# Performance work log

Hardware: AMD Instinct MI355X
Metric: run time of the kernel (lower is better)

## Reference

```python
import jax, jax.numpy as jnp
import numpy as np

B, S, E, H = 4, 2048, 1024, 16
DH = E // H  # head_dim = 64


def setup_inputs() -> dict:
    key = jax.random.key(0)
    k1, k2, k3 = jax.random.split(key, 3)
    x = jax.random.normal(k1, (B, S, E), dtype=jnp.float32)
    # xavier-uniform-like scale for dense kernels
    Wqkv = jax.random.normal(k2, (E, 3 * E), dtype=jnp.float32) * (1.0 / np.sqrt(E))
    Wout = jax.random.normal(k3, (E, E), dtype=jnp.float32) * (1.0 / np.sqrt(E))
    return {"x": x, "Wqkv": Wqkv, "Wout": Wout}


def reference(x, Wqkv, Wout):
    b, s, e = x.shape
    qkv = jnp.einsum("bse,ef->bsf", x, Wqkv)            # [B,S,3E]
    qkv = qkv.reshape(b, s, H, 3 * DH).transpose(0, 2, 1, 3)  # [B,H,S,3*DH]
    q, k, v = jnp.split(qkv, 3, axis=-1)                # each [B,H,S,DH]
    scale = 1.0 / jnp.sqrt(jnp.asarray(DH, dtype=x.dtype))
    scores = jnp.einsum("bhqd,bhkd->bhqk", q, k) * scale  # [B,H,S,S] materialized
    attn = jax.nn.softmax(scores, axis=-1)
    values = jnp.einsum("bhqk,bhkd->bhqd", attn, v)     # [B,H,S,DH]
    values = values.transpose(0, 2, 1, 3).reshape(b, s, e)
    out = jnp.einsum("bse,ef->bsf", values, Wout)       # [B,S,E]
    return out
```

## Files before the change

### kernel.cpp

```cpp
#include <hip/hip_runtime.h>

typedef __attribute__((ext_vector_type(8))) __bf16 bf16x8;
typedef __attribute__((ext_vector_type(4))) float f32x4;

#define LOG2E 1.4426950408889634f
#define QSCALE (0.125f * LOG2E)
#define SMAX_FIXED 13.0f

static __device__ __forceinline__ void gl_lds16(const void* g, void* l) {
  __builtin_amdgcn_global_load_lds(
      (__attribute__((address_space(1))) void*)(g),
      (__attribute__((address_space(3))) void*)(l), 16, 0, 0);
}

__global__ __launch_bounds__(256) void convert_f32_bf16(const float* __restrict__ in,
                                                        __bf16* __restrict__ out,
                                                        int n8) {
  const int i = blockIdx.x * 256 + threadIdx.x;
  if (i >= n8) return;
  const f32x4 a = *(const f32x4*)(in + (size_t)i * 8);
  const f32x4 b = *(const f32x4*)(in + (size_t)i * 8 + 4);
  bf16x8 o;
#pragma unroll
  for (int j = 0; j < 4; ++j) o[j] = (__bf16)a[j];
#pragma unroll
  for (int j = 0; j < 4; ++j) o[4 + j] = (__bf16)b[j];
  *(bf16x8*)(out + (size_t)i * 8) = o;
}

__global__ __launch_bounds__(256) void transpose_f32_bf16(
    const float* __restrict__ in, __bf16* __restrict__ out, int R, int C) {
  __shared__ __bf16 tile[64][72];
  const int t = threadIdx.x;
  const int c0 = blockIdx.x * 64;
  const int r0 = blockIdx.y * 64;
  const int lr = t >> 2;
  const int lc = (t & 3) * 16;
  const float* src = in + (size_t)(r0 + lr) * C + c0 + lc;
  bf16x8 w0, w1;
#pragma unroll
  for (int j = 0; j < 2; ++j) {
    const f32x4 a = *(const f32x4*)(src + j * 8);
    const f32x4 b = *(const f32x4*)(src + j * 8 + 4);
    bf16x8 o;
#pragma unroll
    for (int k = 0; k < 4; ++k) o[k] = (__bf16)a[k];
#pragma unroll
    for (int k = 0; k < 4; ++k) o[4 + k] = (__bf16)b[k];
    *(bf16x8*)&tile[lr][lc + j * 8] = o;
  }
  __syncthreads();
#pragma unroll
  for (int j = 0; j < 8; ++j) {
    w0[j] = tile[lc + j][lr];
    w1[j] = tile[lc + 8 + j][lr];
  }
  __bf16* dst = out + (size_t)(c0 + lr) * R + r0 + lc;
  *(bf16x8*)dst = w0;
  *(bf16x8*)(dst + 8) = w1;
}

#define FENCEOFF

#define STAGE_A(TT, KH)                                                  \
  do {                                                                   \
    const int kg_ = (TT) * 64 + (KH) * 32;                               \
    char* d_ = lds + ((TT) & 1) * 32768 + (KH) * 16384 + t * 16;         \
    gl_lds16(Ab + g0 + kg_, d_);                                         \
    gl_lds16(Ab + g1 + kg_, d_ + 8192);                                  \
  } while (0)

#define STAGE_B(TT, KH)                                                  \
  do {                                                                   \
    const int kg_ = (TT) * 64 + (KH) * 32;                               \
    char* d_ = lds + 65536 + ((TT) & 1) * 32768 + (KH) * 16384 + t * 16; \
    gl_lds16(Bb + g0 + kg_, d_);                                         \
    gl_lds16(Bb + g1 + kg_, d_ + 8192);                                  \
  } while (0)

#define READ_A(MIH, KK)                                                          \
  do {                                                                           \
    const char* p_ = lds + buf * 32768 + (KK) * 16384 +                          \
                     (wm * 8 + (MIH) * 4) * 1024 + lfo;                          \
    a0 = *(const bf16x8*)p_;                                                     \
    a1 = *(const bf16x8*)(p_ + 1024);                                            \
    a2 = *(const bf16x8*)(p_ + 2048);                                            \
    a3 = *(const bf16x8*)(p_ + 3072);                                            \
  } while (0)

#define READ_B(KK)                                                               \
  do {                                                                           \
    const char* p_ = lds + 65536 + buf * 32768 + (KK) * 16384 + wn * 4096 + lfo; \
    b0 = *(const bf16x8*)p_;                                                     \
    b1 = *(const bf16x8*)(p_ + 1024);                                            \
    b2 = *(const bf16x8*)(p_ + 2048);                                            \
    b3 = *(const bf16x8*)(p_ + 3072);                                            \
  } while (0)

#define MROW(H, MI, AV)                                                          \
  acc[(H) * 4 + (MI)][0] =                                                       \
      __builtin_amdgcn_mfma_f32_16x16x32_bf16(AV, b0, acc[(H) * 4 + (MI)][0], 0, 0, 0); \
  acc[(H) * 4 + (MI)][1] =                                                       \
      __builtin_amdgcn_mfma_f32_16x16x32_bf16(AV, b1, acc[(H) * 4 + (MI)][1], 0, 0, 0); \
  acc[(H) * 4 + (MI)][2] =                                                       \
      __builtin_amdgcn_mfma_f32_16x16x32_bf16(AV, b2, acc[(H) * 4 + (MI)][2], 0, 0, 0); \
  acc[(H) * 4 + (MI)][3] =                                                       \
      __builtin_amdgcn_mfma_f32_16x16x32_bf16(AV, b3, acc[(H) * 4 + (MI)][3], 0, 0, 0);

#define MFMA16(H)                      \
  do {                                 \
    __builtin_amdgcn_s_setprio(1);     \
    MROW(H, 0, a0)                     \
    MROW(H, 1, a1)                     \
    MROW(H, 2, a2)                     \
    MROW(H, 3, a3)                     \
    __builtin_amdgcn_s_setprio(0);     \
  } while (0)

template <int EPI>
__global__ __launch_bounds__(512, 2) void gemm256(
    const __bf16* __restrict__ A, const __bf16* __restrict__ Bt,
    float* __restrict__ Cf, __bf16* __restrict__ q_ws, __bf16* __restrict__ k_ws,
    __bf16* __restrict__ vT_ws, int M, int N, int K) {
  (void)M;
  extern __shared__ char lds[];
  const int t = threadIdx.x;
  const int lane = t & 63;
  const int quad = lane >> 4, l15 = lane & 15;
  const int w = t >> 6;
  const int wm = w >> 2, wn = w & 3;

  const int gx = gridDim.x;
  int lid = blockIdx.y * gx + blockIdx.x;
  lid = (lid & 7) * ((gx * gridDim.y) >> 3) + (lid >> 3);
  const int m0 = (lid % gx) * 256;
  const int n0 = (lid / gx) * 256;

  int rowS[2], kcS[2];
#pragma unroll
  for (int l = 0; l < 2; ++l) {
    const int LB = l * 8192 + t * 16;
    const int r_in = (LB >> 6) & 15;
    const int ch = ((LB >> 5) & 1) ^ ((r_in >> 3) & 1);
    rowS[l] = (LB >> 10) * 16 + r_in;
    kcS[l] = ch * 16 + ((LB >> 4) & 1) * 8;
  }
  const __bf16* Ab = A + (size_t)m0 * K;
  const __bf16* Bb = Bt + (size_t)n0 * K;
  const size_t g0 = (size_t)rowS[0] * K + kcS[0];
  const size_t g1 = (size_t)rowS[1] * K + kcS[1];

  const int lfo = l15 * 64 + ((((quad >> 1) ^ (l15 >> 3)) & 1) << 5) + ((quad & 1) << 4);

  const f32x4 fzero = {0.f, 0.f, 0.f, 0.f};
  f32x4 acc[8][4];
#pragma unroll
  for (int i = 0; i < 8; ++i)
#pragma unroll
    for (int j = 0; j < 4; ++j) acc[i][j] = fzero;

  const int nt = K >> 6;
  bf16x8 a0, a1, a2, a3, b0, b1, b2, b3;

  STAGE_A(0, 0);
  STAGE_B(0, 0);
  STAGE_A(0, 1);
  STAGE_B(0, 1);
  if (nt > 1) {
    STAGE_A(1, 0);
    STAGE_B(1, 0);
    asm volatile("s_waitcnt vmcnt(4)");
  } else {
    asm volatile("s_waitcnt vmcnt(0)");
  }
  __builtin_amdgcn_s_barrier();

  for (int tt = 0; tt < nt; ++tt) {
    const int buf = tt & 1;
    READ_A(0, 0);
    READ_B(0);
    if (tt + 1 < nt) STAGE_A(tt + 1, 1);
    __builtin_amdgcn_s_barrier();
    asm volatile("s_waitcnt lgkmcnt(0)");
    MFMA16(0);
    __builtin_amdgcn_s_barrier();
    READ_A(1, 0);
    if (tt + 1 < nt) STAGE_B(tt + 1, 1);
    __builtin_amdgcn_s_barrier();
    asm volatile("s_waitcnt lgkmcnt(0)");
    MFMA16(1);
    __builtin_amdgcn_s_barrier();
    READ_A(0, 1);
    READ_B(1);
    if (tt + 2 < nt) STAGE_A(tt + 2, 0);
    __builtin_amdgcn_s_barrier();
    asm volatile("s_waitcnt lgkmcnt(0)");
    MFMA16(0);
    __builtin_amdgcn_s_barrier();
    READ_A(1, 1);
    if (tt + 2 < nt) STAGE_B(tt + 2, 0);
    __builtin_amdgcn_s_barrier();
    asm volatile("s_waitcnt lgkmcnt(0)");
    MFMA16(1);
    if (tt + 2 < nt)
      asm volatile("s_waitcnt vmcnt(4)");
    else
      asm volatile("s_waitcnt vmcnt(0)");
    __builtin_amdgcn_s_barrier();
  }

#pragma unroll
  for (int mi = 0; mi < 8; ++mi) {
#pragma unroll
    for (int r = 0; r < 4; ++r) {
      const int row = m0 + wm * 128 + mi * 16 + quad * 4 + r;
#pragma unroll
      for (int ni = 0; ni < 4; ++ni) {
        const int col = n0 + wn * 64 + ni * 16 + l15;
        const float v = acc[mi][ni][r];
        if (EPI == 0) {
          const int b = row >> 11, s = row & 2047;
          const int h = col / 192;
          const int rr = col - h * 192;
          const int ty = rr >> 6, d = rr & 63;
          const int bh = b * 16 + h;
          if (ty == 0)
            q_ws[((size_t)bh * 2048 + s) * 64 + d] = (__bf16)v;
          else if (ty == 1)
            k_ws[((size_t)bh * 2048 + s) * 64 + d] = (__bf16)v;
          else
            vT_ws[((size_t)bh * 64 + d) * 2048 + s] = (__bf16)v;
        } else {
          Cf[(size_t)row * N + col] = v;
        }
      }
    }
  }
}

__global__ __launch_bounds__(256) void flash_attn(
    const __bf16* __restrict__ q_ws, const __bf16* __restrict__ k_ws,
    const __bf16* __restrict__ vT_ws, __bf16* __restrict__ values) {
  __shared__ __bf16 sK[64][72];
  __shared__ __bf16 sVt[64][72];
  __shared__ __bf16 sP[4][32][72];
  const int t = threadIdx.x;
  const int lane = t & 63, w = t >> 6, quad = lane >> 4, l15 = lane & 15;
  const int qt = blockIdx.x;
  const int bh = blockIdx.y;
  const __bf16* Qb = q_ws + (size_t)bh * 2048 * 64;
  const __bf16* Kb = k_ws + (size_t)bh * 2048 * 64;
  const __bf16* Vtb = vT_ws + (size_t)bh * 64 * 2048;
  const int qrow0 = qt * 128 + w * 32;

  bf16x8 qf[2][2];
#pragma unroll
  for (int mi = 0; mi < 2; ++mi)
#pragma unroll
    for (int ks = 0; ks < 2; ++ks)
      qf[mi][ks] = *(const bf16x8*)(Qb + (size_t)(qrow0 + mi * 16 + l15) * 64 +
                                    ks * 32 + quad * 8);

  bf16x8 ones;
#pragma unroll
  for (int j = 0; j < 8; ++j) ones[j] = (__bf16)1.0f;

  const f32x4 fzero = {0.f, 0.f, 0.f, 0.f};
  f32x4 accO[2][4];
  f32x4 accL[2];
#pragma unroll
  for (int mi = 0; mi < 2; ++mi) {
    accL[mi] = fzero;
#pragma unroll
    for (int ni = 0; ni < 4; ++ni) accO[mi][ni] = fzero;
  }

  const int srow = t >> 2;
  const int scol = (t & 3) * 16;

  bf16x8 ka, kb2, va, vb;
  {
    const __bf16* ks0 = Kb + (size_t)srow * 64 + scol;
    ka = *(const bf16x8*)ks0;
    kb2 = *(const bf16x8*)(ks0 + 8);
    const __bf16* vs0 = Vtb + (size_t)srow * 2048 + scol;
    va = *(const bf16x8*)vs0;
    vb = *(const bf16x8*)(vs0 + 8);
  }

  for (int kt = 0; kt < 32; ++kt) {
    *(bf16x8*)&sK[srow][scol] = ka;
    *(bf16x8*)&sK[srow][scol + 8] = kb2;
    *(bf16x8*)&sVt[srow][scol] = va;
    *(bf16x8*)&sVt[srow][scol + 8] = vb;
    __syncthreads();

    if (kt < 31) {
      const __bf16* ksn = Kb + (size_t)((kt + 1) * 64 + srow) * 64 + scol;
      ka = *(const bf16x8*)ksn;
      kb2 = *(const bf16x8*)(ksn + 8);
      const __bf16* vsn = Vtb + (size_t)srow * 2048 + (kt + 1) * 64 + scol;
      va = *(const bf16x8*)vsn;
      vb = *(const bf16x8*)(vsn + 8);
    }

    f32x4 accS[2][4];
#pragma unroll
    for (int mi = 0; mi < 2; ++mi)
#pragma unroll
      for (int ni = 0; ni < 4; ++ni) accS[mi][ni] = fzero;
#pragma unroll
    for (int ks = 0; ks < 2; ++ks) {
      bf16x8 kf[4];
#pragma unroll
      for (int ni = 0; ni < 4; ++ni)
        kf[ni] = *(const bf16x8*)&sK[ni * 16 + l15][ks * 32 + quad * 8];
#pragma unroll
      for (int mi = 0; mi < 2; ++mi)
#pragma unroll
        for (int ni = 0; ni < 4; ++ni)
          accS[mi][ni] = __builtin_amdgcn_mfma_f32_16x16x32_bf16(
              qf[mi][ks], kf[ni], accS[mi][ni], 0, 0, 0);
    }

#pragma unroll
    for (int mi = 0; mi < 2; ++mi) {
#pragma unroll
      for (int r = 0; r < 4; ++r) {
        const int prow = mi * 16 + quad * 4 + r;
#pragma unroll
        for (int ni = 0; ni < 4; ++ni) {
          const float p =
              __builtin_amdgcn_exp2f(accS[mi][ni][r] * QSCALE - SMAX_FIXED);
          sP[w][prow][ni * 16 + l15] = (__bf16)p;
        }
      }
    }
    __threadfence_block();

#pragma unroll
    for (int ks = 0; ks < 2; ++ks) {
      bf16x8 vf[4], pf[2];
#pragma unroll
      for (int ni = 0; ni < 4; ++ni)
        vf[ni] = *(const bf16x8*)&sVt[ni * 16 + l15][ks * 32 + quad * 8];
#pragma unroll
      for (int mi = 0; mi < 2; ++mi)
        pf[mi] = *(const bf16x8*)&sP[w][mi * 16 + l15][ks * 32 + quad * 8];
#pragma unroll
      for (int mi = 0; mi < 2; ++mi) {
#pragma unroll
        for (int ni = 0; ni < 4; ++ni)
          accO[mi][ni] = __builtin_amdgcn_mfma_f32_16x16x32_bf16(
              pf[mi], vf[ni], accO[mi][ni], 0, 0, 0);
        accL[mi] = __builtin_amdgcn_mfma_f32_16x16x32_bf16(pf[mi], ones, accL[mi],
                                                           0, 0, 0);
      }
    }
    __syncthreads();
  }

  const int b = bh >> 4, h = bh & 15;
#pragma unroll
  for (int mi = 0; mi < 2; ++mi) {
#pragma unroll
    for (int r = 0; r < 4; ++r) {
      const float inv = 1.0f / accL[mi][r];
      const int s = qrow0 + mi * 16 + quad * 4 + r;
#pragma unroll
      for (int ni = 0; ni < 4; ++ni)
        values[((size_t)(b * 2048 + s)) * 1024 + h * 64 + ni * 16 + l15] =
            (__bf16)(accO[mi][ni][r] * inv);
    }
  }
}

extern "C" void kernel_launch(void* const* d_in, const int* in_sizes, int n_in,
                              void* d_out, int out_size, void* d_ws, size_t ws_size,
                              hipStream_t stream) {
  (void)out_size; (void)ws_size;
  float* out = (float*)d_out;
  char* wsb = (char*)d_ws;
  __bf16* xb = (__bf16*)(wsb + 256);
  __bf16* WqkvT = xb + 8388608;
  __bf16* WoutT = WqkvT + 3145728;
  __bf16* q_ws = WoutT + 1048576;
  __bf16* k_ws = q_ws + 8388608;
  __bf16* vT_ws = k_ws + 8388608;
  __bf16* values = xb;

  const float *px = (const float*)d_in[0], *pw = (const float*)d_in[1],
              *po = (const float*)d_in[2];
  for (int i = 0; i < n_in; ++i) {
    if (in_sizes[i] == 8388608) px = (const float*)d_in[i];
    else if (in_sizes[i] == 3145728) pw = (const float*)d_in[i];
    else if (in_sizes[i] == 1048576) po = (const float*)d_in[i];
  }

  hipFuncSetAttribute(reinterpret_cast<const void*>(&gemm256<0>),
                      hipFuncAttributeMaxDynamicSharedMemorySize, 131072);
  hipFuncSetAttribute(reinterpret_cast<const void*>(&gemm256<1>),
                      hipFuncAttributeMaxDynamicSharedMemorySize, 131072);

  convert_f32_bf16<<<4096, 256, 0, stream>>>(px, xb, 1048576);
  transpose_f32_bf16<<<dim3(48, 16), 256, 0, stream>>>(pw, WqkvT, 1024, 3072);
  transpose_f32_bf16<<<dim3(16, 16), 256, 0, stream>>>(po, WoutT, 1024, 1024);
  gemm256<0><<<dim3(32, 12), 512, 131072, stream>>>(xb, WqkvT, nullptr, q_ws, k_ws,
                                                    vT_ws, 8192, 3072, 1024);
  flash_attn<<<dim3(16, 64), 256, 0, stream>>>(q_ws, k_ws, vT_ws, values);
  gemm256<1><<<dim3(32, 4), 512, 131072, stream>>>(values, WoutT, out, nullptr,
                                                   nullptr, nullptr, 8192, 1024, 1024);
}
```

Measured before the change: 314.7 us.

## Swizzle flash-attention LDS layout and transpose V in a separate pass

The QKV GEMM epilogue now writes V row-major into the output buffer, used as scratch, and a new transpose kernel produces V^T, replacing the strided scattered stores that wrote V^T directly. In flash attention, the K, V^T and P tiles in LDS move to a swizzled byte layout with XOR on 32-byte halves to avoid bank conflicts on the MFMA fragment reads. MFMA blocks are also wrapped in s_setprio. This adds an extra kernel launch and an extra round trip of V through memory.

```diff
diff --git a/kernel.cpp b/kernel.cpp
--- a/kernel.cpp
+++ b/kernel.cpp
@@ -60,7 +60,28 @@
   *(bf16x8*)(dst + 8) = w1;
 }
 
-#define FENCEOFF
+__global__ __launch_bounds__(256) void transpose_v(const __bf16* __restrict__ v,
+                                                   __bf16* __restrict__ vT) {
+  __shared__ __bf16 tile[64][72];
+  const int t = threadIdx.x;
+  const int s0 = blockIdx.x * 64;
+  const int bh = blockIdx.y;
+  const int lr = t >> 2, lc = (t & 3) * 16;
+  const __bf16* src = v + ((size_t)bh * 2048 + s0 + lr) * 64 + lc;
+  *(bf16x8*)&tile[lr][lc] = *(const bf16x8*)src;
+  *(bf16x8*)&tile[lr][lc + 8] = *(const bf16x8*)(src + 8);
+  __syncthreads();
+  bf16x8 w0, w1;
+#pragma unroll
+  for (int j = 0; j < 8; ++j) {
+    w0[j] = tile[lc + j][lr];
+    w1[j] = tile[lc + 8 + j][lr];
+  }
+  __bf16* dst = vT + ((size_t)bh * 64 + lr) * 2048 + s0 + lc;
+  *(bf16x8*)dst = w0;
+  *(bf16x8*)(dst + 8) = w1;
+}
+
 
 #define STAGE_A(TT, KH)                                                  \
   do {                                                                   \
@@ -121,7 +142,7 @@
 __global__ __launch_bounds__(512, 2) void gemm256(
     const __bf16* __restrict__ A, const __bf16* __restrict__ Bt,
     float* __restrict__ Cf, __bf16* __restrict__ q_ws, __bf16* __restrict__ k_ws,
-    __bf16* __restrict__ vT_ws, int M, int N, int K) {
+    __bf16* __restrict__ v_ws, int M, int N, int K) {
   (void)M;
   extern __shared__ char lds[];
   const int t = threadIdx.x;
@@ -229,7 +250,7 @@
           else if (ty == 1)
             k_ws[((size_t)bh * 2048 + s) * 64 + d] = (__bf16)v;
           else
-            vT_ws[((size_t)bh * 64 + d) * 2048 + s] = (__bf16)v;
+            v_ws[((size_t)bh * 2048 + s) * 64 + d] = (__bf16)v;
         } else {
           Cf[(size_t)row * N + col] = v;
         }
@@ -241,9 +262,9 @@
 __global__ __launch_bounds__(256) void flash_attn(
     const __bf16* __restrict__ q_ws, const __bf16* __restrict__ k_ws,
     const __bf16* __restrict__ vT_ws, __bf16* __restrict__ values) {
-  __shared__ __bf16 sK[64][72];
-  __shared__ __bf16 sVt[64][72];
-  __shared__ __bf16 sP[4][32][72];
+  __shared__ __align__(16) char sK[8192];
+  __shared__ __align__(16) char sVt[8192];
+  __shared__ __align__(16) char sP[4][4096];
   const int t = threadIdx.x;
   const int lane = t & 63, w = t >> 6, quad = lane >> 4, l15 = lane & 15;
   const int qt = blockIdx.x;
@@ -275,6 +296,12 @@
     for (int ni = 0; ni < 4; ++ni) accO[mi][ni] = fzero;
   }
 
+  const int lfo = l15 * 64 + ((((quad >> 1) ^ (l15 >> 3)) & 1) << 5) + ((quad & 1) << 4);
+  const int wrow = t >> 2;
+  const int tc = t & 3;
+  const int wofs = ((tc >> 1) << 12) + ((wrow >> 4) << 10) + ((wrow & 15) << 6) +
+                   (((tc & 1) ^ ((wrow >> 3) & 1)) << 5);
+
   const int srow = t >> 2;
   const int scol = (t & 3) * 16;
 
@@ -289,10 +316,10 @@
   }
 
   for (int kt = 0; kt < 32; ++kt) {
-    *(bf16x8*)&sK[srow][scol] = ka;
-    *(bf16x8*)&sK[srow][scol + 8] = kb2;
-    *(bf16x8*)&sVt[srow][scol] = va;
-    *(bf16x8*)&sVt[srow][scol + 8] = vb;
+    *(bf16x8*)(sK + wofs) = ka;
+    *(bf16x8*)(sK + wofs + 16) = kb2;
+    *(bf16x8*)(sVt + wofs) = va;
+    *(bf16x8*)(sVt + wofs + 16) = vb;
     __syncthreads();
 
     if (kt < 31) {
@@ -314,25 +341,28 @@
       bf16x8 kf[4];
 #pragma unroll
       for (int ni = 0; ni < 4; ++ni)
-        kf[ni] = *(const bf16x8*)&sK[ni * 16 + l15][ks * 32 + quad * 8];
+        kf[ni] = *(const bf16x8*)(sK + ks * 4096 + ni * 1024 + lfo);
+      __builtin_amdgcn_s_setprio(1);
 #pragma unroll
       for (int mi = 0; mi < 2; ++mi)
 #pragma unroll
         for (int ni = 0; ni < 4; ++ni)
           accS[mi][ni] = __builtin_amdgcn_mfma_f32_16x16x32_bf16(
               qf[mi][ks], kf[ni], accS[mi][ni], 0, 0, 0);
+      __builtin_amdgcn_s_setprio(0);
     }
 
 #pragma unroll
     for (int mi = 0; mi < 2; ++mi) {
 #pragma unroll
       for (int r = 0; r < 4; ++r) {
-        const int prow = mi * 16 + quad * 4 + r;
 #pragma unroll
         for (int ni = 0; ni < 4; ++ni) {
           const float p =
               __builtin_amdgcn_exp2f(accS[mi][ni][r] * QSCALE - SMAX_FIXED);
-          sP[w][prow][ni * 16 + l15] = (__bf16)p;
+          *(__bf16*)(sP[w] + ((ni >> 1) << 11) + (mi << 10) +
+                     ((quad * 4 + r) << 6) + (((ni & 1) ^ (quad >> 1)) << 5) +
+                     (l15 << 1)) = (__bf16)p;
         }
       }
     }
@@ -343,10 +373,11 @@
       bf16x8 vf[4], pf[2];
 #pragma unroll
       for (int ni = 0; ni < 4; ++ni)
-        vf[ni] = *(const bf16x8*)&sVt[ni * 16 + l15][ks * 32 + quad * 8];
+        vf[ni] = *(const bf16x8*)(sVt + ks * 4096 + ni * 1024 + lfo);
 #pragma unroll
       for (int mi = 0; mi < 2; ++mi)
-        pf[mi] = *(const bf16x8*)&sP[w][mi * 16 + l15][ks * 32 + quad * 8];
+        pf[mi] = *(const bf16x8*)(sP[w] + ks * 2048 + mi * 1024 + lfo);
+      __builtin_amdgcn_s_setprio(1);
 #pragma unroll
       for (int mi = 0; mi < 2; ++mi) {
 #pragma unroll
@@ -356,6 +387,7 @@
         accL[mi] = __builtin_amdgcn_mfma_f32_16x16x32_bf16(pf[mi], ones, accL[mi],
                                                            0, 0, 0);
       }
+      __builtin_amdgcn_s_setprio(0);
     }
     __syncthreads();
   }
@@ -388,6 +420,7 @@
   __bf16* k_ws = q_ws + 8388608;
   __bf16* vT_ws = k_ws + 8388608;
   __bf16* values = xb;
+  __bf16* v_rows = (__bf16*)d_out;
 
   const float *px = (const float*)d_in[0], *pw = (const float*)d_in[1],
               *po = (const float*)d_in[2];
@@ -406,7 +439,8 @@
   transpose_f32_bf16<<<dim3(48, 16), 256, 0, stream>>>(pw, WqkvT, 1024, 3072);
   transpose_f32_bf16<<<dim3(16, 16), 256, 0, stream>>>(po, WoutT, 1024, 1024);
   gemm256<0><<<dim3(32, 12), 512, 131072, stream>>>(xb, WqkvT, nullptr, q_ws, k_ws,
-                                                    vT_ws, 8192, 3072, 1024);
+                                                    v_rows, 8192, 3072, 1024);
+  transpose_v<<<dim3(32, 64), 256, 0, stream>>>(v_rows, vT_ws);
   flash_attn<<<dim3(16, 64), 256, 0, stream>>>(q_ws, k_ws, vT_ws, values);
   gemm256<1><<<dim3(32, 4), 512, 131072, stream>>>(values, WoutT, out, nullptr,
                                                    nullptr, nullptr, 8192, 1024, 1024);
```

New measurement: 338.8 us. +7.7%, slower.
